# Performance work log

Hardware: AMD Instinct MI355X
Metric: run time of the kernel (lower is better)

## Reference

```python
import jax, jax.numpy as jnp
import numpy as np

EMB = 64
HID = 1024
SEQ = 9
BATCH = 4096


def setup_inputs() -> dict:
    key = jax.random.key(0)
    ks = jax.random.split(key, 10)
    s = lambda *sh: 1.0 / np.sqrt(sh[-1])
    return {
        "observed": jax.random.normal(ks[0], (SEQ, BATCH, 2), dtype=jnp.float32),
        "W_emb": jax.random.normal(ks[1], (EMB, 2), dtype=jnp.float32) * s(2),
        "b_emb": jnp.zeros((EMB,), dtype=jnp.float32),
        "W_ih": jax.random.normal(ks[2], (4 * HID, EMB), dtype=jnp.float32) * s(EMB),
        "b_ih": jnp.zeros((4 * HID,), dtype=jnp.float32),
        "W_hh": jax.random.normal(ks[3], (4 * HID, HID), dtype=jnp.float32) * s(HID),
        "b_hh": jnp.zeros((4 * HID,), dtype=jnp.float32),
        "W_out": jax.random.normal(ks[4], (5, HID), dtype=jnp.float32) * s(HID),
        "b_out": jnp.zeros((5,), dtype=jnp.float32),
        "n_predict": 12,
    }


def _cell(x, h, c, W_ih, b_ih, W_hh, b_hh):
    # torch.nn.LSTMCell gate math, gate order i, f, g, o
    gates = x @ W_ih.T + b_ih + h @ W_hh.T + b_hh  # [B, 4H]
    i, f, g, o = jnp.split(gates, 4, axis=-1)
    c_new = jax.nn.sigmoid(f) * c + jax.nn.sigmoid(i) * jnp.tanh(g)
    h_new = jax.nn.sigmoid(o) * jnp.tanh(c_new)
    return h_new, c_new


def reference(observed, W_emb, b_emb, W_ih, b_ih, W_hh, b_hh, W_out, b_out, n_predict):
    B = observed.shape[1]
    H = W_hh.shape[1]
    h0 = jnp.zeros((B, H), dtype=observed.dtype)
    c0 = jnp.zeros((B, H), dtype=observed.dtype)

    diffs = observed[1:] - observed[:-1]  # [SEQ-1, B, 2]

    def obs_step(carry, d):
        h, c = carry
        emb = jax.nn.relu(d @ W_emb.T + b_emb)  # [B, EMB]
        h, c = _cell(emb, h, c, W_ih, b_ih, W_hh, b_hh)
        normal = h @ W_out.T + b_out  # [B, 5]
        return (h, c), normal

    (h, c), normals_obs = jax.lax.scan(obs_step, (h0, c0), diffs)
    new_vel = normals_obs[-1][:, :2]

    def pred_step(carry, _):
        h, c, nv = carry
        emb = jax.nn.relu(jax.lax.stop_gradient(nv) @ W_emb.T + b_emb)
        h, c = _cell(emb, h, c, W_ih, b_ih, W_hh, b_hh)
        normal = h @ W_out.T + b_out
        return (h, c, normal[:, :2]), normal

    (_, _, _), normals_pred = jax.lax.scan(
        pred_step, (h, c, new_vel), None, length=n_predict - 1)

    # training-mode output: stacked raw 'normal' params, shape [SEQ-1+n_predict-1, B, 5]
    return jnp.concatenate([normals_obs, normals_pred], axis=0)
```

## Files before the change

kernel.cpp:

```cpp
#include <hip/hip_runtime.h>
#include <stdint.h>
#include <stddef.h>

#define BATCH 4096
#define HID   1024
#define EMB   64
#define NKH   32
#define NSTEP 19
#define NOBS  8
#define WSL   139264

typedef _Float16 f16;
typedef _Float16 half8 __attribute__((ext_vector_type(8)));
typedef float    float4v __attribute__((ext_vector_type(4)));

__device__ __forceinline__ float sigm(float x) { return 1.f / (1.f + __expf(-x)); }
__device__ __forceinline__ float tanh_f(float x) { return 1.f - 2.f / (__expf(2.f * x) + 1.f); }

__global__ void pack_kernel(const float* __restrict__ W_ih, const float* __restrict__ b_ih,
                            const float* __restrict__ W_hh, const float* __restrict__ b_hh,
                            f16* __restrict__ Wsw, float* __restrict__ bc) {
  int gid = blockIdx.x * blockDim.x + threadIdx.x;
  int tt = gid / WSL;
  int rem = gid - tt * WSL;
  int kt = rem >> 12;
  int ni = (rem >> 9) & 7;
  int lane = (rem >> 3) & 63;
  int e = rem & 7;
  int p = tt * 128 + ni * 16 + (lane & 15);
  int g = (p >> 4) & 3;
  int u = (p >> 8) * 64 + ((p >> 6) & 3) * 16 + (p & 15);
  int orig = g * HID + u;
  int k = kt * 32 + ((lane >> 4) << 3) + e;
  float val = (k < EMB) ? W_ih[orig * EMB + k] : W_hh[orig * HID + (k - EMB)];
  Wsw[gid] = (f16)val;
  if (k == 0) bc[p] = b_ih[orig] + b_hh[orig];
}

__global__ __launch_bounds__(512, 4)
void gemm_cell_kernel(const f16* __restrict__ Xp, const f16* __restrict__ Wsw,
                      const float* __restrict__ bc,
                      f16* __restrict__ c_ws, f16* __restrict__ Xn,
                      float* __restrict__ po_ws, const float* __restrict__ W_out,
                      const float* __restrict__ obs_t, const float* __restrict__ outprev,
                      int mode, const float* __restrict__ W_emb,
                      const float* __restrict__ b_emb) {
  __shared__ f16 smem[24576];

  const int tid = threadIdx.x;
  const int lane = tid & 63;
  const int w = tid >> 6;
  const int l15 = lane & 15;
  const int quad = lane >> 4;
  const int wm = w >> 2, wn = w & 3;
  const int sh = wn >> 1, nq = wn & 1;

  const int id = blockIdx.x;
  const int x = id & 7, rr0 = id >> 3;
  const int bn = x * 2 + (rr0 & 1);
  const int bm = rr0 >> 1;
  const int slice = bn * 2 + sh;

  float4v acc[4][4];
#pragma unroll
  for (int mi = 0; mi < 4; ++mi)
#pragma unroll
    for (int ni = 0; ni < 4; ++ni) acc[mi][ni] = (float4v){0.f, 0.f, 0.f, 0.f};

  half8 R[3];

  auto gload = [&](int kh) {
#pragma unroll
    for (int i = 0; i < 3; ++i) {
      const int c = w * 3 + i;
      if (c < 8) {
        R[i] = *(const half8*)(Xp + ((size_t)(bm * 8 + c) * NKH + kh) * 512 + lane * 8);
      } else {
        const int cb = c - 8;
        R[i] = *(const half8*)(Wsw + (size_t)(bn * 2 + (cb >> 3)) * WSL +
                               (size_t)(2 + kh) * 4096 + (cb & 7) * 512 + lane * 8);
      }
    }
  };
  auto dswr = [&](int p2) {
    f16* buf = smem + p2 * 12288;
#pragma unroll
    for (int i = 0; i < 3; ++i)
      *(half8*)(buf + (w * 3 + i) * 512 + lane * 8) = R[i];
  };
  auto compute = [&](const f16* base) {
    half8 bq[4];
#pragma unroll
    for (int ni = 0; ni < 4; ++ni)
      bq[ni] = *(const half8*)(base + 4096 + (sh * 8 + nq * 4 + ni) * 512 + lane * 8);
    __builtin_amdgcn_s_setprio(1);
#pragma unroll
    for (int mi = 0; mi < 4; ++mi) {
      half8 am = *(const half8*)(base + (wm * 4 + mi) * 512 + lane * 8);
#pragma unroll
      for (int ni = 0; ni < 4; ++ni)
        acc[mi][ni] = __builtin_amdgcn_mfma_f32_16x16x32_f16(am, bq[ni], acc[mi][ni], 0, 0, 0);
    }
    __builtin_amdgcn_s_setprio(0);
  };

  if (mode != 0) gload(0);

  {
    float d0[4], d1[4];
#pragma unroll
    for (int mi = 0; mi < 4; ++mi) {
      const int row = (bm * 8 + wm * 4 + mi) * 16 + l15;
      if (mode <= 1) {
        const float* o = obs_t + (size_t)row * 2;
        d0[mi] = o[BATCH * 2] - o[0];
        d1[mi] = o[BATCH * 2 + 1] - o[1];
      } else {
        d0[mi] = outprev[(size_t)row * 5 + 0];
        d1[mi] = outprev[(size_t)row * 5 + 1];
      }
    }
#pragma unroll
    for (int kt = 0; kt < 2; ++kt) {
      float w0[8], w1[8], be[8];
#pragma unroll
      for (int e = 0; e < 8; ++e) {
        const int j = kt * 32 + quad * 8 + e;
        w0[e] = W_emb[2 * j];
        w1[e] = W_emb[2 * j + 1];
        be[e] = b_emb[j];
      }
      half8 bfe[4];
#pragma unroll
      for (int ni = 0; ni < 4; ++ni)
        bfe[ni] = *(const half8*)(Wsw + (size_t)slice * WSL + kt * 4096 + (nq * 4 + ni) * 512 + lane * 8);
#pragma unroll
      for (int mi = 0; mi < 4; ++mi) {
        half8 ae;
#pragma unroll
        for (int e = 0; e < 8; ++e)
          ae[e] = (f16)fmaxf(d0[mi] * w0[e] + d1[mi] * w1[e] + be[e], 0.f);
#pragma unroll
        for (int ni = 0; ni < 4; ++ni)
          acc[mi][ni] = __builtin_amdgcn_mfma_f32_16x16x32_f16(ae, bfe[ni], acc[mi][ni], 0, 0, 0);
      }
    }
  }

  if (mode != 0) {
    dswr(0);
    gload(1);
    asm volatile("s_waitcnt lgkmcnt(0)" ::: "memory");
    __builtin_amdgcn_sched_barrier(0);
    __builtin_amdgcn_s_barrier();
    for (int s = 1; s <= 32; ++s) {
      if (s < 32) dswr(s & 1);
      if (s < 31) gload(s + 1);
      compute(smem + ((s - 1) & 1) * 12288);
      asm volatile("s_waitcnt lgkmcnt(0)" ::: "memory");
      __builtin_amdgcn_sched_barrier(0);
      __builtin_amdgcn_s_barrier();
    }
  }

  float bb[4];
#pragma unroll
  for (int ni = 0; ni < 4; ++ni) bb[ni] = bc[bn * 256 + wn * 64 + ni * 16 + l15];
  const int u = bn * 64 + wn * 16 + l15;
  float wo[5];
#pragma unroll
  for (int o = 0; o < 5; ++o) wo[o] = W_out[o * HID + u];

  f16* cbase = c_ws + ((size_t)(bm * 16 + bn) * 512 + tid) * 16;
  half8 cv[2];
  if (mode != 0) {
#pragma unroll
    for (int q = 0; q < 2; ++q) cv[q] = *(const half8*)(cbase + q * 8);
  }

  __syncthreads();
  float* pol = (float*)smem;

#pragma unroll
  for (int mi = 0; mi < 4; ++mi) {
#pragma unroll
    for (int r = 0; r < 4; ++r) {
      const int rl = wm * 64 + mi * 16 + quad * 4 + r;
      const int row = bm * 128 + rl;
      const int ci = mi * 4 + r;
      float gi = acc[mi][0][r] + bb[0];
      float gf = acc[mi][1][r] + bb[1];
      float gg = acc[mi][2][r] + bb[2];
      float go = acc[mi][3][r] + bb[3];
      float co = (mode == 0) ? 0.f : (float)cv[ci >> 3][ci & 7];
      float cn = sigm(gf) * co + sigm(gi) * tanh_f(gg);
      cv[ci >> 3][ci & 7] = (f16)cn;
      float h = sigm(go) * tanh_f(cn);
      Xn[(((size_t)(row >> 4) * NKH + slice) * 64 + (quad * 4 + r) +
          16 * ((wn & 1) * 2 + (l15 >> 3))) * 8 + (l15 & 7)] = (f16)h;
      float pa[5];
#pragma unroll
      for (int o = 0; o < 5; ++o) pa[o] = h * wo[o];
#pragma unroll
      for (int o = 0; o < 5; ++o) {
        pa[o] += __shfl_xor(pa[o], 1, 64);
        pa[o] += __shfl_xor(pa[o], 2, 64);
        pa[o] += __shfl_xor(pa[o], 4, 64);
        pa[o] += __shfl_xor(pa[o], 8, 64);
      }
      if (l15 == 0) {
#pragma unroll
        for (int o = 0; o < 5; ++o) pol[(rl * 4 + wn) * 5 + o] = pa[o];
      }
    }
  }
#pragma unroll
  for (int q = 0; q < 2; ++q) *(half8*)(cbase + q * 8) = cv[q];

  __syncthreads();
  for (int idx = tid; idx < 640; idx += 512) {
    const int rl = idx / 5, o = idx - rl * 5;
    float s = 0.f;
#pragma unroll
    for (int j = 0; j < 4; ++j) s += pol[(rl * 4 + j) * 5 + o];
    po_ws[((size_t)bn * BATCH + bm * 128 + rl) * 5 + o] = s;
  }
}

__global__ __launch_bounds__(256)
void reduce_kernel(const float* __restrict__ po_ws, const float* __restrict__ b_out,
                   float* __restrict__ out_t) {
  const int tid = threadIdx.x;
  const int r0 = blockIdx.x * 32;
  if (tid < 160) {
    const int rowl = tid / 5, o = tid - rowl * 5;
    const int row = r0 + rowl;
    float s = 0.f;
#pragma unroll
    for (int g = 0; g < 16; ++g) s += po_ws[((size_t)g * BATCH + row) * 5 + o];
    out_t[(size_t)row * 5 + o] = s + b_out[o];
  }
}

extern "C" void kernel_launch(void* const* d_in, const int* in_sizes, int n_in,
                              void* d_out, int out_size, void* d_ws, size_t ws_size,
                              hipStream_t stream) {
  const float* observed = (const float*)d_in[0];
  const float* W_emb = (const float*)d_in[1];
  const float* b_emb = (const float*)d_in[2];
  const float* W_ih = (const float*)d_in[3];
  const float* b_ih = (const float*)d_in[4];
  const float* W_hh = (const float*)d_in[5];
  const float* b_hh = (const float*)d_in[6];
  const float* W_out = (const float*)d_in[7];
  const float* b_out = (const float*)d_in[8];
  float* out = (float*)d_out;

  uint8_t* ws = (uint8_t*)d_ws;
  const size_t WSW_BYTES = (size_t)32 * WSL * sizeof(f16);
  const size_t XH_BYTES = (size_t)256 * NKH * 64 * 8 * sizeof(f16);
  f16* Wsw = (f16*)ws;
  float* bc = (float*)(ws + WSW_BYTES);
  f16* X0 = (f16*)(ws + WSW_BYTES + 16384);
  f16* X1 = (f16*)(ws + WSW_BYTES + 16384 + XH_BYTES);
  f16* c_ws = (f16*)(ws + WSW_BYTES + 16384 + 2 * XH_BYTES);
  float* po_ws = (float*)(ws + WSW_BYTES + 16384 + 2 * XH_BYTES + (size_t)BATCH * HID * 2);

  pack_kernel<<<(32 * WSL) / 256, 256, 0, stream>>>(W_ih, b_ih, W_hh, b_hh, Wsw, bc);

  for (int t = 0; t < NSTEP; ++t) {
    f16* Xc = (t & 1) ? X1 : X0;
    f16* Xq = (t & 1) ? X0 : X1;
    const int mode = (t == 0) ? 0 : (t < NOBS ? 1 : 2);
    gemm_cell_kernel<<<512, 512, 0, stream>>>(
        Xq, Wsw, bc, c_ws, Xc, po_ws, W_out,
        observed + (size_t)t * BATCH * 2, out + (size_t)(t - 1) * BATCH * 5,
        mode, W_emb, b_emb);
    reduce_kernel<<<BATCH / 32, 256, 0, stream>>>(po_ws, b_out, out + (size_t)t * BATCH * 5);
  }
}
```

Before: 1.247 ms.

## Drop LDS staging in gate GEMM and load MFMA fragments directly from global

Rewrites the fused LSTM gate GEMM so each wave loads its A (hidden state) and B (packed weights) fragments straight from global memory into registers. A two-stage register double buffer replaces the LDS double buffer and its per-k-step barriers. Blocks shrink from 512 to 256 threads covering 64 batch rows instead of 128, so the grid doubles and the c-state and partial-output indexing is adjusted to match. This removes LDS traffic and synchronisation, but the four waves of a block now each fetch the same A tile, which leans on L1/L2 and raises register pressure.

Result: faster. 1.135 ms (-9.0%).

```diff
diff --git a/kernel.cpp b/kernel.cpp
--- a/kernel.cpp
+++ b/kernel.cpp
@@ -37,7 +37,7 @@
   if (k == 0) bc[p] = b_ih[orig] + b_hh[orig];
 }
 
-__global__ __launch_bounds__(512, 4)
+__global__ __launch_bounds__(256, 3)
 void gemm_cell_kernel(const f16* __restrict__ Xp, const f16* __restrict__ Wsw,
                       const float* __restrict__ bc,
                       f16* __restrict__ c_ws, f16* __restrict__ Xn,
@@ -45,14 +45,13 @@
                       const float* __restrict__ obs_t, const float* __restrict__ outprev,
                       int mode, const float* __restrict__ W_emb,
                       const float* __restrict__ b_emb) {
-  __shared__ f16 smem[24576];
+  __shared__ float pol[64 * 4 * 5];
 
   const int tid = threadIdx.x;
   const int lane = tid & 63;
-  const int w = tid >> 6;
+  const int wn = tid >> 6;
   const int l15 = lane & 15;
   const int quad = lane >> 4;
-  const int wm = w >> 2, wn = w & 3;
   const int sh = wn >> 1, nq = wn & 1;
 
   const int id = blockIdx.x;
@@ -67,50 +66,14 @@
 #pragma unroll
     for (int ni = 0; ni < 4; ++ni) acc[mi][ni] = (float4v){0.f, 0.f, 0.f, 0.f};
 
-  half8 R[3];
-
-  auto gload = [&](int kh) {
-#pragma unroll
-    for (int i = 0; i < 3; ++i) {
-      const int c = w * 3 + i;
-      if (c < 8) {
-        R[i] = *(const half8*)(Xp + ((size_t)(bm * 8 + c) * NKH + kh) * 512 + lane * 8);
-      } else {
-        const int cb = c - 8;
-        R[i] = *(const half8*)(Wsw + (size_t)(bn * 2 + (cb >> 3)) * WSL +
-                               (size_t)(2 + kh) * 4096 + (cb & 7) * 512 + lane * 8);
-      }
-    }
-  };
-  auto dswr = [&](int p2) {
-    f16* buf = smem + p2 * 12288;
-#pragma unroll
-    for (int i = 0; i < 3; ++i)
-      *(half8*)(buf + (w * 3 + i) * 512 + lane * 8) = R[i];
-  };
-  auto compute = [&](const f16* base) {
-    half8 bq[4];
-#pragma unroll
-    for (int ni = 0; ni < 4; ++ni)
-      bq[ni] = *(const half8*)(base + 4096 + (sh * 8 + nq * 4 + ni) * 512 + lane * 8);
-    __builtin_amdgcn_s_setprio(1);
-#pragma unroll
-    for (int mi = 0; mi < 4; ++mi) {
-      half8 am = *(const half8*)(base + (wm * 4 + mi) * 512 + lane * 8);
-#pragma unroll
-      for (int ni = 0; ni < 4; ++ni)
-        acc[mi][ni] = __builtin_amdgcn_mfma_f32_16x16x32_f16(am, bq[ni], acc[mi][ni], 0, 0, 0);
-    }
-    __builtin_amdgcn_s_setprio(0);
-  };
-
-  if (mode != 0) gload(0);
+  const f16* aB = Xp + (size_t)(bm * 4) * (NKH * 512) + lane * 8;
+  const f16* bB = Wsw + (size_t)slice * WSL + (size_t)2 * 4096 + (nq * 4) * 512 + lane * 8;
 
   {
     float d0[4], d1[4];
 #pragma unroll
     for (int mi = 0; mi < 4; ++mi) {
-      const int row = (bm * 8 + wm * 4 + mi) * 16 + l15;
+      const int row = (bm * 4 + mi) * 16 + l15;
       if (mode <= 1) {
         const float* o = obs_t + (size_t)row * 2;
         d0[mi] = o[BATCH * 2] - o[0];
@@ -148,19 +111,33 @@
   }
 
   if (mode != 0) {
-    dswr(0);
-    gload(1);
-    asm volatile("s_waitcnt lgkmcnt(0)" ::: "memory");
-    __builtin_amdgcn_sched_barrier(0);
-    __builtin_amdgcn_s_barrier();
-    for (int s = 1; s <= 32; ++s) {
-      if (s < 32) dswr(s & 1);
-      if (s < 31) gload(s + 1);
-      compute(smem + ((s - 1) & 1) * 12288);
-      asm volatile("s_waitcnt lgkmcnt(0)" ::: "memory");
-      __builtin_amdgcn_sched_barrier(0);
-      __builtin_amdgcn_s_barrier();
-    }
+    half8 afA[4], bfA[4], afB[4], bfB[4];
+#define LOADF(af, bf, kh)                                                      \
+  do {                                                                         \
+    _Pragma("unroll") for (int mi = 0; mi < 4; ++mi)                           \
+        af[mi] = *(const half8*)(aB + mi * (NKH * 512) + (kh) * 512);          \
+    _Pragma("unroll") for (int ni = 0; ni < 4; ++ni)                           \
+        bf[ni] = *(const half8*)(bB + (size_t)(kh) * 4096 + ni * 512);         \
+  } while (0)
+#define MFMA_ALL(af, bf)                                                       \
+  do {                                                                         \
+    __builtin_amdgcn_s_setprio(1);                                             \
+    _Pragma("unroll") for (int mi = 0; mi < 4; ++mi)                           \
+    _Pragma("unroll") for (int ni = 0; ni < 4; ++ni)                           \
+        acc[mi][ni] =                                                          \
+            __builtin_amdgcn_mfma_f32_16x16x32_f16(af[mi], bf[ni], acc[mi][ni], 0, 0, 0); \
+    __builtin_amdgcn_s_setprio(0);                                             \
+  } while (0)
+    LOADF(afA, bfA, 0);
+    for (int i = 0; i < NKH / 2; ++i) {
+      const int k1 = 2 * i + 1;
+      LOADF(afB, bfB, k1);
+      MFMA_ALL(afA, bfA);
+      if (k1 + 1 < NKH) LOADF(afA, bfA, k1 + 1);
+      MFMA_ALL(afB, bfB);
+    }
+#undef LOADF
+#undef MFMA_ALL
   }
 
   float bb[4];
@@ -171,22 +148,19 @@
 #pragma unroll
   for (int o = 0; o < 5; ++o) wo[o] = W_out[o * HID + u];
 
-  f16* cbase = c_ws + ((size_t)(bm * 16 + bn) * 512 + tid) * 16;
+  f16* cbase = c_ws + ((size_t)(bm * 16 + bn) * 256 + tid) * 16;
   half8 cv[2];
   if (mode != 0) {
 #pragma unroll
     for (int q = 0; q < 2; ++q) cv[q] = *(const half8*)(cbase + q * 8);
   }
 
-  __syncthreads();
-  float* pol = (float*)smem;
-
 #pragma unroll
   for (int mi = 0; mi < 4; ++mi) {
 #pragma unroll
     for (int r = 0; r < 4; ++r) {
-      const int rl = wm * 64 + mi * 16 + quad * 4 + r;
-      const int row = bm * 128 + rl;
+      const int rl = mi * 16 + quad * 4 + r;
+      const int row = bm * 64 + rl;
       const int ci = mi * 4 + r;
       float gi = acc[mi][0][r] + bb[0];
       float gf = acc[mi][1][r] + bb[1];
@@ -218,12 +192,12 @@
   for (int q = 0; q < 2; ++q) *(half8*)(cbase + q * 8) = cv[q];
 
   __syncthreads();
-  for (int idx = tid; idx < 640; idx += 512) {
+  for (int idx = tid; idx < 320; idx += 256) {
     const int rl = idx / 5, o = idx - rl * 5;
     float s = 0.f;
 #pragma unroll
     for (int j = 0; j < 4; ++j) s += pol[(rl * 4 + j) * 5 + o];
-    po_ws[((size_t)bn * BATCH + bm * 128 + rl) * 5 + o] = s;
+    po_ws[((size_t)bn * BATCH + bm * 64 + rl) * 5 + o] = s;
   }
 }
 
@@ -272,7 +246,7 @@
     f16* Xc = (t & 1) ? X1 : X0;
     f16* Xq = (t & 1) ? X0 : X1;
     const int mode = (t == 0) ? 0 : (t < NOBS ? 1 : 2);
-    gemm_cell_kernel<<<512, 512, 0, stream>>>(
+    gemm_cell_kernel<<<1024, 256, 0, stream>>>(
         Xq, Wsw, bc, c_ws, Xc, po_ws, W_out,
         observed + (size_t)t * BATCH * 2, out + (size_t)(t - 1) * BATCH * 5,
         mode, W_emb, b_emb);
```
